# Performance work log

Hardware: AMD Instinct MI355X
Metric: run time of the kernel (lower is better)

## Reference

```python
import jax, jax.numpy as jnp
import numpy as np

N_NODES = 100000
N_EDGES = 1600000
D_IN = 128
D_OUT = 128
BN_EPS = 1e-5


def setup_inputs() -> dict:
    key = jax.random.key(0)
    ks = jax.random.split(key, 6)
    x = jax.random.normal(ks[0], (N_NODES, D_IN), dtype=jnp.float32)
    edge_index = jax.random.randint(ks[1], (2, N_EDGES), 0, N_NODES, dtype=jnp.int32)
    edge_weight = jax.random.uniform(ks[2], (N_EDGES,), dtype=jnp.float32)
    W = jax.random.normal(ks[3], (D_IN, D_OUT), dtype=jnp.float32) / np.sqrt(D_IN)
    b = jax.random.normal(ks[4], (D_OUT,), dtype=jnp.float32) * 0.01
    gamma = jnp.ones((D_OUT,), dtype=jnp.float32)
    beta = jnp.zeros((D_OUT,), dtype=jnp.float32)
    return {"x": x, "edge_index": edge_index, "edge_weight": edge_weight,
            "W": W, "b": b, "gamma": gamma, "beta": beta}


def reference(x, edge_index, edge_weight, W, b, gamma, beta):
    n = x.shape[0]
    # add self loops (add_self_loops=True)
    self_loops = jnp.arange(n, dtype=edge_index.dtype)
    row = jnp.concatenate([edge_index[0], self_loops])  # source
    col = jnp.concatenate([edge_index[1], self_loops])  # destination
    ew = jnp.concatenate([edge_weight, jnp.ones((n,), x.dtype)])
    # degree via scatter-add of ones on source nodes
    deg = jax.ops.segment_sum(jnp.ones_like(ew), row, num_segments=n)
    dinv = jnp.where(deg > 0, jax.lax.rsqrt(deg), 0.0)
    norm = dinv[row] * dinv[col] * ew  # [E+N]
    # linear transform
    h = x @ W + b  # [N, D_OUT]
    # per-edge gather -> scale -> scatter-add (vectorized form of the python loop)
    msgs = norm[:, None] * h[row]  # [E+N, D_OUT]
    out = jax.ops.segment_sum(msgs, col, num_segments=n)  # [N, D_OUT]
    # BatchNorm1d (training mode: biased batch stats)
    mean = jnp.mean(out, axis=0)
    var = jnp.mean(jnp.square(out - mean), axis=0)
    out = (out - mean) * jax.lax.rsqrt(var + BN_EPS) * gamma + beta
    return jax.nn.relu(out)
```

## Files before the change

kernel.cpp:

```cpp
#include <hip/hip_runtime.h>

#define DD 128
#define CAP 64
#define BINCAP 4608
#define S1_EPB 7168
#define DEG_R 16384
#define DEG_S 8

typedef __attribute__((ext_vector_type(8))) short short8;
typedef __attribute__((ext_vector_type(4))) float f32x4;

__device__ __forceinline__ unsigned short f2bf(float f) {
    unsigned int u; __builtin_memcpy(&u, &f, 4);
    unsigned int r = (u + 0x7FFFu + ((u >> 16) & 1u)) >> 16;
    return (unsigned short)r;
}
__device__ __forceinline__ unsigned int pack_bf(float a, float b) {
    return (unsigned int)f2bf(a) | ((unsigned int)f2bf(b) << 16);
}
__device__ __forceinline__ float lo_bf(unsigned int p) {
    unsigned int u = (p & 0xFFFFu) << 16; float f; __builtin_memcpy(&f, &u, 4); return f;
}
__device__ __forceinline__ float hi_bf(unsigned int p) {
    unsigned int u = p & 0xFFFF0000u; float f; __builtin_memcpy(&f, &u, 4); return f;
}
__device__ __forceinline__ float i2f(int v) { float f; __builtin_memcpy(&f, &v, 4); return f; }
__device__ __forceinline__ int f2i(float v) { int i; __builtin_memcpy(&i, &v, 4); return i; }

__global__ void k_init(int* deg, int* cursor, float* colsumR, float* colsumsqR, int N, int NBIN) {
    int i = blockIdx.x * 256 + threadIdx.x;
    if (i < N) deg[i] = 1;
    if (i < NBIN) cursor[i] = 0;
    if (i < 1024) { colsumR[i] = 0.0f; colsumsqR[i] = 0.0f; }
}

__global__ void k_wprep(const float* __restrict__ W, unsigned short* __restrict__ Wfrag) {
    int i = blockIdx.x * 256 + threadIdx.x;
    int k = i >> 7, n = i & 127;
    int tt = n >> 4, s = k >> 5, l = (((k >> 3) & 3) << 4) | (n & 15), j = k & 7;
    Wfrag[((tt * 4 + s) * 64 + l) * 8 + j] = f2bf(W[k * DD + n]);
}

__global__ __launch_bounds__(1024) void k_fused(
    const int* __restrict__ ei, const float* __restrict__ ew,
    int* __restrict__ deg, int* __restrict__ cursor, long long* __restrict__ coarse,
    int E, int N, int NBIN, int nS1i, int nDeg,
    const float* __restrict__ x, const unsigned short* __restrict__ Wfrag,
    const float* __restrict__ b, unsigned short* __restrict__ h)
{
    __shared__ int smem[16384];
    int t = threadIdx.x;
    int id = blockIdx.x;
    int role, rid;
    if (id < 2 * nS1i)           { role = (id & 1); rid = id >> 1; }
    else if (id < 2 * nS1i + nDeg) { role = 2; rid = id - 2 * nS1i; }
    else                         { role = 1; rid = nS1i + (id - 2 * nS1i - nDeg); }

    const int* row = ei;
    const int* col = ei + E;

    if (role == 0) {
        int* scnt  = smem;
        int* soff  = smem + 512;
        int* gbase = smem + 1024;
        long long* sorted = (long long*)(smem + 1536);
        for (int i = t; i < 512; i += 1024) scnt[i] = 0;
        __syncthreads();
        int e0 = rid * S1_EPB;
        int myrank[7];
#pragma unroll
        for (int j = 0; j < 7; ++j) {
            int e = e0 + j * 1024 + t;
            if (e < E) myrank[j] = atomicAdd(&scnt[col[e] >> 8], 1);
        }
        __syncthreads();
        if (t < 512) soff[t] = scnt[t];
        __syncthreads();
        for (int off = 1; off < 512; off <<= 1) {
            int v = 0;
            if (t < 512 && t >= off) v = soff[t - off];
            __syncthreads();
            if (t < 512) soff[t] += v;
            __syncthreads();
        }
        if (t < NBIN && scnt[t] > 0) gbase[t] = atomicAdd(&cursor[t], scnt[t]);
#pragma unroll
        for (int j = 0; j < 7; ++j) {
            int e = e0 + j * 1024 + t;
            if (e < E) {
                int c = col[e];
                int bn = c >> 8;
                int lo = row[e] | ((c & 255) << 17);
                long long ent = ((long long)(unsigned)f2i(ew[e]) << 32) | (unsigned)lo;
                sorted[(soff[bn] - scnt[bn]) + myrank[j]] = ent;
            }
        }
        __syncthreads();
        int wave = t >> 6, lane = t & 63;
        for (int bn = wave; bn < NBIN; bn += 16) {
            int k = scnt[bn];
            if (k == 0) continue;
            int off0 = soff[bn] - k;
            int gb = gbase[bn];
            long long* dst = coarse + (size_t)bn * BINCAP;
            for (int j = lane; j < k; j += 64) {
                int gp = gb + j;
                if (gp < BINCAP) dst[gp] = sorted[off0 + j];
            }
        }
        return;
    }
    if (role == 2) {
        int nr = (N + DEG_R - 1) / DEG_R;
        int ri = rid % nr, si = rid / nr;
        int* lc = smem;
        for (int i = t; i < DEG_R; i += 1024) lc[i] = 0;
        __syncthreads();
        int base = ri * DEG_R;
        int per = (E + DEG_S - 1) / DEG_S;
        int es = si * per, ee = es + per; if (ee > E) ee = E;
        int q0 = es >> 2, q1 = ee >> 2;
        const int4* r4 = (const int4*)row;
        for (int q = q0 + t; q < q1; q += 1024) {
            int4 v = r4[q];
            unsigned d0 = (unsigned)(v.x - base), d1 = (unsigned)(v.y - base);
            unsigned d2 = (unsigned)(v.z - base), d3 = (unsigned)(v.w - base);
            if (d0 < DEG_R) atomicAdd(&lc[d0], 1);
            if (d1 < DEG_R) atomicAdd(&lc[d1], 1);
            if (d2 < DEG_R) atomicAdd(&lc[d2], 1);
            if (d3 < DEG_R) atomicAdd(&lc[d3], 1);
        }
        for (int e = (q1 << 2) + t; e < ee; e += 1024) {
            unsigned d = (unsigned)(row[e] - base);
            if (d < DEG_R) atomicAdd(&lc[d], 1);
        }
        __syncthreads();
        for (int i = t; i < DEG_R; i += 1024) {
            int node = base + i, k = lc[i];
            if (node < N && k) atomicAdd(&deg[node], k);
        }
        return;
    }
    int lane = t & 63, wave = t >> 6;
    int row0 = rid * 256 + wave * 16;
    int mrow = row0 + (lane & 15);
    int kgrp = lane >> 4;
    f32x4 acc[8];
#pragma unroll
    for (int i = 0; i < 8; ++i) acc[i] = (f32x4){0.f, 0.f, 0.f, 0.f};
    const short8* Wf = (const short8*)Wfrag;
#pragma unroll
    for (int s = 0; s < 4; ++s) {
        float xv[8];
        if (mrow < N) {
            const float4* xp = (const float4*)(x + (size_t)mrow * DD + s * 32 + kgrp * 8);
            float4 xa = xp[0], xb = xp[1];
            xv[0] = xa.x; xv[1] = xa.y; xv[2] = xa.z; xv[3] = xa.w;
            xv[4] = xb.x; xv[5] = xb.y; xv[6] = xb.z; xv[7] = xb.w;
        } else {
#pragma unroll
            for (int j = 0; j < 8; ++j) xv[j] = 0.f;
        }
        short8 af;
#pragma unroll
        for (int j = 0; j < 8; ++j) af[j] = (short)f2bf(xv[j]);
#pragma unroll
        for (int tt = 0; tt < 8; ++tt) {
            short8 bf = Wf[(tt * 4 + s) * 64 + lane];
            acc[tt] = __builtin_amdgcn_mfma_f32_16x16x32_bf16(af, bf, acc[tt], 0, 0, 0);
        }
    }
    int drow = row0 + (lane >> 4) * 4;
    int coll = lane & 15;
#pragma unroll
    for (int tt = 0; tt < 8; ++tt) {
        int cc = tt * 16 + coll;
        float bias = b[cc];
#pragma unroll
        for (int rr = 0; rr < 4; ++rr) {
            int rw = drow + rr;
            if (rw < N) h[(size_t)rw * DD + cc] = f2bf(acc[tt][rr] + bias);
        }
    }
}

__global__ __launch_bounds__(1024) void k_stage2(
    const long long* __restrict__ coarse, const int* __restrict__ cursor,
    long long* __restrict__ bucket, int* __restrict__ cnt, int N)
{
    __shared__ int fcnt[256], fpos[256], fcur[256];
    __shared__ long long sorted2[BINCAP];
    int bn = blockIdx.x, t = threadIdx.x;
    int m = cursor[bn]; if (m > BINCAP) m = BINCAP;
    for (int i = t; i < 256; i += 1024) fcnt[i] = 0;
    __syncthreads();
    const long long* src = coarse + (size_t)bn * BINCAP;
    for (int i = t; i < m; i += 1024) {
        int lo = (int)src[i];
        atomicAdd(&fcnt[(lo >> 17) & 255], 1);
    }
    __syncthreads();
    if (t < 256) fpos[t] = fcnt[t];
    __syncthreads();
    for (int off = 1; off < 256; off <<= 1) {
        int v = 0;
        if (t < 256 && t >= off) v = fpos[t - off];
        __syncthreads();
        if (t < 256) fpos[t] += v;
        __syncthreads();
    }
    if (t < 256) fcur[t] = fpos[t] - fcnt[t];
    __syncthreads();
    for (int i = t; i < m; i += 1024) {
        long long v = src[i];
        int clo = ((int)v >> 17) & 255;
        int p = atomicAdd(&fcur[clo], 1);
        sorted2[p] = v;
    }
    __syncthreads();
    int wave = t >> 6, lane = t & 63;
    for (int d = wave; d < 256; d += 16) {
        int c = (bn << 8) + d;
        if (c >= N) continue;
        int k = fcnt[d]; if (k > CAP) k = CAP;
        int off0 = fpos[d] - fcnt[d];
        for (int j = lane; j < k; j += 64)
            bucket[(size_t)c * CAP + j] = sorted2[off0 + j];
    }
    if (t < 256) {
        int c = (bn << 8) + t;
        if (c < N) { int k = fcnt[t]; cnt[c] = (k > CAP) ? CAP : k; }
    }
}

__global__ __launch_bounds__(1024) void k_aggregate(
    const unsigned int* __restrict__ h, const int* __restrict__ cnt,
    const int2* __restrict__ bucket, const int* __restrict__ deg,
    unsigned int* __restrict__ outb, float* __restrict__ colsumR,
    float* __restrict__ colsumsqR, int N)
{
    __shared__ float ls[2048], lq[2048];
    int t = threadIdx.x, wave = t >> 6, lane = t & 63;
    int gw = blockIdx.x * 16 + wave;
    float s0 = 0, s1 = 0, q0 = 0, q1 = 0;
    for (int n = gw; n < N; n += 512 * 16) {
        float dn = rsqrtf((float)deg[n]);
        unsigned int p = h[(size_t)n * 64 + lane];
        float a0 = dn * lo_bf(p), a1 = dn * hi_bf(p);
        int cn = cnt[n];
        const int2* bk = bucket + (size_t)n * CAP;
        int j = 0;
        for (; j + 8 <= cn; j += 8) {
            int2 d0 = bk[j],     d1 = bk[j + 1], d2 = bk[j + 2], d3 = bk[j + 3];
            int2 d4 = bk[j + 4], d5 = bk[j + 5], d6 = bk[j + 6], d7 = bk[j + 7];
            int s0_ = d0.x & 0x1FFFF, s1_ = d1.x & 0x1FFFF, s2_ = d2.x & 0x1FFFF, s3_ = d3.x & 0x1FFFF;
            int s4_ = d4.x & 0x1FFFF, s5_ = d5.x & 0x1FFFF, s6_ = d6.x & 0x1FFFF, s7_ = d7.x & 0x1FFFF;
            unsigned int g0 = h[(size_t)s0_ * 64 + lane];
            unsigned int g1 = h[(size_t)s1_ * 64 + lane];
            unsigned int g2 = h[(size_t)s2_ * 64 + lane];
            unsigned int g3 = h[(size_t)s3_ * 64 + lane];
            unsigned int g4 = h[(size_t)s4_ * 64 + lane];
            unsigned int g5 = h[(size_t)s5_ * 64 + lane];
            unsigned int g6 = h[(size_t)s6_ * 64 + lane];
            unsigned int g7 = h[(size_t)s7_ * 64 + lane];
            float w0 = rsqrtf((float)deg[s0_]) * i2f(d0.y), w1 = rsqrtf((float)deg[s1_]) * i2f(d1.y);
            float w2 = rsqrtf((float)deg[s2_]) * i2f(d2.y), w3 = rsqrtf((float)deg[s3_]) * i2f(d3.y);
            float w4 = rsqrtf((float)deg[s4_]) * i2f(d4.y), w5 = rsqrtf((float)deg[s5_]) * i2f(d5.y);
            float w6 = rsqrtf((float)deg[s6_]) * i2f(d6.y), w7 = rsqrtf((float)deg[s7_]) * i2f(d7.y);
            a0 = fmaf(w0, lo_bf(g0), a0); a1 = fmaf(w0, hi_bf(g0), a1);
            a0 = fmaf(w1, lo_bf(g1), a0); a1 = fmaf(w1, hi_bf(g1), a1);
            a0 = fmaf(w2, lo_bf(g2), a0); a1 = fmaf(w2, hi_bf(g2), a1);
            a0 = fmaf(w3, lo_bf(g3), a0); a1 = fmaf(w3, hi_bf(g3), a1);
            a0 = fmaf(w4, lo_bf(g4), a0); a1 = fmaf(w4, hi_bf(g4), a1);
            a0 = fmaf(w5, lo_bf(g5), a0); a1 = fmaf(w5, hi_bf(g5), a1);
            a0 = fmaf(w6, lo_bf(g6), a0); a1 = fmaf(w6, hi_bf(g6), a1);
            a0 = fmaf(w7, lo_bf(g7), a0); a1 = fmaf(w7, hi_bf(g7), a1);
        }
        for (; j < cn; ++j) {
            int2 d = bk[j];
            int sr = d.x & 0x1FFFF;
            unsigned int g = h[(size_t)sr * 64 + lane];
            float w = rsqrtf((float)deg[sr]) * i2f(d.y);
            a0 = fmaf(w, lo_bf(g), a0);
            a1 = fmaf(w, hi_bf(g), a1);
        }
        a0 *= dn; a1 *= dn;
        outb[(size_t)n * 64 + lane] = pack_bf(a0, a1);
        s0 += a0; q0 += a0 * a0;
        s1 += a1; q1 += a1 * a1;
    }
    ls[wave * 128 + lane * 2] = s0; ls[wave * 128 + lane * 2 + 1] = s1;
    lq[wave * 128 + lane * 2] = q0; lq[wave * 128 + lane * 2 + 1] = q1;
    __syncthreads();
    if (t < 128) {
        float S = 0, Q = 0;
#pragma unroll
        for (int w = 0; w < 16; ++w) { S += ls[w * 128 + t]; Q += lq[w * 128 + t]; }
        int rep = (blockIdx.x & 7) * 128 + t;
        atomicAdd(&colsumR[rep], S);
        atomicAdd(&colsumsqR[rep], Q);
    }
}

__global__ void k_bn_final(const float* __restrict__ colsumR, const float* __restrict__ colsumsqR,
                           const float* __restrict__ gamma, const float* __restrict__ beta,
                           float* __restrict__ ss, int N) {
    int c = threadIdx.x;
    float S = 0, Q = 0;
#pragma unroll
    for (int r = 0; r < 8; ++r) { S += colsumR[r * 128 + c]; Q += colsumsqR[r * 128 + c]; }
    float invN = 1.0f / (float)N;
    float mean = S * invN;
    float var = Q * invN - mean * mean;
    float inv = rsqrtf(var + 1e-5f);
    float sc = gamma[c] * inv;
    ss[c] = sc;
    ss[128 + c] = beta[c] - mean * sc;
}

__global__ __launch_bounds__(256) void k_bn_apply(const unsigned int* __restrict__ outb,
                                                  float* __restrict__ out,
                                                  const float* __restrict__ ss, int total64) {
    int i = blockIdx.x * 256 + threadIdx.x;
    if (i >= total64) return;
    int c0 = (i & 63) * 2;
    unsigned int p = outb[i];
    float v0 = fmaxf(lo_bf(p) * ss[c0]     + ss[128 + c0],     0.0f);
    float v1 = fmaxf(hi_bf(p) * ss[c0 + 1] + ss[128 + c0 + 1], 0.0f);
    ((float2*)out)[i] = make_float2(v0, v1);
}

extern "C" void kernel_launch(void* const* d_in, const int* in_sizes, int n_in,
                              void* d_out, int out_size, void* d_ws, size_t ws_size,
                              hipStream_t stream) {
    const float* x     = (const float*)d_in[0];
    const int* ei      = (const int*)d_in[1];
    const float* ew    = (const float*)d_in[2];
    const float* W     = (const float*)d_in[3];
    const float* b     = (const float*)d_in[4];
    const float* gamma = (const float*)d_in[5];
    const float* beta  = (const float*)d_in[6];
    float* out = (float*)d_out;

    int N = in_sizes[0] / DD;
    int E = in_sizes[2];
    int NBIN = (N + 255) / 256;

    char* wsb = (char*)d_ws;
    size_t off = 0;
    auto alloc = [&](size_t bytes) -> char* {
        char* p = wsb + off;
        off = (off + bytes + 255) & ~(size_t)255;
        return p;
    };
    int* deg        = (int*)alloc((size_t)N * 4);
    int* cnt        = (int*)alloc((size_t)N * 4);
    int* cursor     = (int*)alloc((size_t)NBIN * 4);
    long long* coarse = (long long*)alloc((size_t)NBIN * BINCAP * 8);
    long long* bucket = (long long*)alloc((size_t)N * CAP * 8);
    unsigned short* h = (unsigned short*)alloc((size_t)N * DD * 2);
    unsigned short* Wfrag = (unsigned short*)alloc(DD * DD * 2);
    unsigned int* outb = (unsigned int*)alloc((size_t)N * 64 * 4);
    float* colsumR   = (float*)alloc(1024 * 4);
    float* colsumsqR = (float*)alloc(1024 * 4);
    float* ss        = (float*)alloc(256 * 4);

    int nS1   = (E + S1_EPB - 1) / S1_EPB;
    int nGemm = (N + 255) / 256;
    int nS1i  = (nS1 < nGemm) ? nS1 : nGemm;
    int nDeg  = ((N + DEG_R - 1) / DEG_R) * DEG_S;
    int GF    = 2 * nS1i + nDeg + (nGemm - nS1i);

    k_init<<<dim3((N + 255) / 256), dim3(256), 0, stream>>>(deg, cursor, colsumR, colsumsqR, N, NBIN);
    k_wprep<<<dim3(64), dim3(256), 0, stream>>>(W, Wfrag);
    k_fused<<<dim3(GF), dim3(1024), 0, stream>>>(ei, ew, deg, cursor, coarse, E, N, NBIN,
                                                 nS1i, nDeg, x, Wfrag, b, h);
    k_stage2<<<dim3(NBIN), dim3(1024), 0, stream>>>(coarse, cursor, bucket, cnt, N);
    k_aggregate<<<dim3(512), dim3(1024), 0, stream>>>((const unsigned int*)h, cnt,
                                                      (const int2*)bucket, deg,
                                                      outb, colsumR, colsumsqR, N);
    k_bn_final<<<dim3(1), dim3(128), 0, stream>>>(colsumR, colsumsqR, gamma, beta, ss, N);
    k_bn_apply<<<dim3((N * 64 + 255) / 256), dim3(256), 0, stream>>>(outb, out, ss, N * 64);
}
```

Measured before the change: 272.9 us.

## Fuse bin sort into aggregation, precompute edge norms, merge prep and BN kernels

The second-stage bin sort now feeds aggregation directly from shared memory, so the per-node bucket array is no longer written to and reread from global memory. The full edge normalisation is computed once per edge during the sort, and the per-node CAP truncation is gone. The init and W-prep kernels are merged into one, as are BN finalize and apply, cutting launch count. In exchange, aggregation parallelism drops to one block per 256-node bin, about 391 blocks, and each block uses much more shared memory, which may lower occupancy and worsen load balance.

```diff
diff --git a/kernel.cpp b/kernel.cpp
--- a/kernel.cpp
+++ b/kernel.cpp
@@ -1,7 +1,6 @@
 #include <hip/hip_runtime.h>
 
 #define DD 128
-#define CAP 64
 #define BINCAP 4608
 #define S1_EPB 7168
 #define DEG_R 16384
@@ -27,15 +26,17 @@
 __device__ __forceinline__ float i2f(int v) { float f; __builtin_memcpy(&f, &v, 4); return f; }
 __device__ __forceinline__ int f2i(float v) { int i; __builtin_memcpy(&i, &v, 4); return i; }
 
-__global__ void k_init(int* deg, int* cursor, float* colsumR, float* colsumsqR, int N, int NBIN) {
-    int i = blockIdx.x * 256 + threadIdx.x;
-    if (i < N) deg[i] = 1;
-    if (i < NBIN) cursor[i] = 0;
-    if (i < 1024) { colsumR[i] = 0.0f; colsumsqR[i] = 0.0f; }
-}
-
-__global__ void k_wprep(const float* __restrict__ W, unsigned short* __restrict__ Wfrag) {
-    int i = blockIdx.x * 256 + threadIdx.x;
+__global__ void k_prep(int* deg, int* cursor, float* colsumR, float* colsumsqR, int N, int NBIN,
+                       int nInit, const float* __restrict__ W, unsigned short* __restrict__ Wfrag) {
+    int bid = blockIdx.x, t = threadIdx.x;
+    if (bid < nInit) {
+        int i = bid * 256 + t;
+        if (i < N) deg[i] = 1;
+        if (i < NBIN) cursor[i] = 0;
+        if (i < 1024) { colsumR[i] = 0.0f; colsumsqR[i] = 0.0f; }
+        return;
+    }
+    int i = (bid - nInit) * 256 + t;
     int k = i >> 7, n = i & 127;
     int tt = n >> 4, s = k >> 5, l = (((k >> 3) & 3) << 4) | (n & 15), j = k & 7;
     Wfrag[((tt * 4 + s) * 64 + l) * 8 + j] = f2bf(W[k * DD + n]);
@@ -184,12 +185,15 @@
     }
 }
 
-__global__ __launch_bounds__(1024) void k_stage2(
+__global__ __launch_bounds__(1024) void k_agg(
     const long long* __restrict__ coarse, const int* __restrict__ cursor,
-    long long* __restrict__ bucket, int* __restrict__ cnt, int N)
+    const int* __restrict__ deg, const unsigned int* __restrict__ h,
+    unsigned int* __restrict__ outb, float* __restrict__ colsumR,
+    float* __restrict__ colsumsqR, int N)
 {
+    __shared__ long long sorted2[BINCAP];
     __shared__ int fcnt[256], fpos[256], fcur[256];
-    __shared__ long long sorted2[BINCAP];
+    __shared__ float ls[2048], lq[2048];
     int bn = blockIdx.x, t = threadIdx.x;
     int m = cursor[bn]; if (m > BINCAP) m = BINCAP;
     for (int i = t; i < 256; i += 1024) fcnt[i] = 0;
@@ -213,60 +217,43 @@
     __syncthreads();
     for (int i = t; i < m; i += 1024) {
         long long v = src[i];
-        int clo = ((int)v >> 17) & 255;
+        int lo = (int)v;
+        int clo = (lo >> 17) & 255;
+        int sr = lo & 0x1FFFF;
+        int c = (bn << 8) + clo;
+        float w = rsqrtf((float)deg[sr]) * rsqrtf((float)deg[c]) * i2f((int)(v >> 32));
         int p = atomicAdd(&fcur[clo], 1);
-        sorted2[p] = v;
+        sorted2[p] = ((long long)(unsigned)f2i(w) << 32) | (unsigned)sr;
     }
     __syncthreads();
     int wave = t >> 6, lane = t & 63;
+    float s0 = 0, s1 = 0, q0 = 0, q1 = 0;
+    const int2* sp = (const int2*)sorted2;
     for (int d = wave; d < 256; d += 16) {
         int c = (bn << 8) + d;
         if (c >= N) continue;
-        int k = fcnt[d]; if (k > CAP) k = CAP;
-        int off0 = fpos[d] - fcnt[d];
-        for (int j = lane; j < k; j += 64)
-            bucket[(size_t)c * CAP + j] = sorted2[off0 + j];
-    }
-    if (t < 256) {
-        int c = (bn << 8) + t;
-        if (c < N) { int k = fcnt[t]; cnt[c] = (k > CAP) ? CAP : k; }
-    }
-}
-
-__global__ __launch_bounds__(1024) void k_aggregate(
-    const unsigned int* __restrict__ h, const int* __restrict__ cnt,
-    const int2* __restrict__ bucket, const int* __restrict__ deg,
-    unsigned int* __restrict__ outb, float* __restrict__ colsumR,
-    float* __restrict__ colsumsqR, int N)
-{
-    __shared__ float ls[2048], lq[2048];
-    int t = threadIdx.x, wave = t >> 6, lane = t & 63;
-    int gw = blockIdx.x * 16 + wave;
-    float s0 = 0, s1 = 0, q0 = 0, q1 = 0;
-    for (int n = gw; n < N; n += 512 * 16) {
-        float dn = rsqrtf((float)deg[n]);
-        unsigned int p = h[(size_t)n * 64 + lane];
-        float a0 = dn * lo_bf(p), a1 = dn * hi_bf(p);
-        int cn = cnt[n];
-        const int2* bk = bucket + (size_t)n * CAP;
+        float dn = rsqrtf((float)deg[c]);
+        float sn = dn * dn;
+        unsigned int p = h[(size_t)c * 64 + lane];
+        float a0 = sn * lo_bf(p), a1 = sn * hi_bf(p);
+        int cn = fcnt[d];
+        int off0 = fpos[d] - cn;
         int j = 0;
         for (; j + 8 <= cn; j += 8) {
-            int2 d0 = bk[j],     d1 = bk[j + 1], d2 = bk[j + 2], d3 = bk[j + 3];
-            int2 d4 = bk[j + 4], d5 = bk[j + 5], d6 = bk[j + 6], d7 = bk[j + 7];
-            int s0_ = d0.x & 0x1FFFF, s1_ = d1.x & 0x1FFFF, s2_ = d2.x & 0x1FFFF, s3_ = d3.x & 0x1FFFF;
-            int s4_ = d4.x & 0x1FFFF, s5_ = d5.x & 0x1FFFF, s6_ = d6.x & 0x1FFFF, s7_ = d7.x & 0x1FFFF;
-            unsigned int g0 = h[(size_t)s0_ * 64 + lane];
-            unsigned int g1 = h[(size_t)s1_ * 64 + lane];
-            unsigned int g2 = h[(size_t)s2_ * 64 + lane];
-            unsigned int g3 = h[(size_t)s3_ * 64 + lane];
-            unsigned int g4 = h[(size_t)s4_ * 64 + lane];
-            unsigned int g5 = h[(size_t)s5_ * 64 + lane];
-            unsigned int g6 = h[(size_t)s6_ * 64 + lane];
-            unsigned int g7 = h[(size_t)s7_ * 64 + lane];
-            float w0 = rsqrtf((float)deg[s0_]) * i2f(d0.y), w1 = rsqrtf((float)deg[s1_]) * i2f(d1.y);
-            float w2 = rsqrtf((float)deg[s2_]) * i2f(d2.y), w3 = rsqrtf((float)deg[s3_]) * i2f(d3.y);
-            float w4 = rsqrtf((float)deg[s4_]) * i2f(d4.y), w5 = rsqrtf((float)deg[s5_]) * i2f(d5.y);
-            float w6 = rsqrtf((float)deg[s6_]) * i2f(d6.y), w7 = rsqrtf((float)deg[s7_]) * i2f(d7.y);
+            int2 d0 = sp[off0 + j],     d1 = sp[off0 + j + 1];
+            int2 d2 = sp[off0 + j + 2], d3 = sp[off0 + j + 3];
+            int2 d4 = sp[off0 + j + 4], d5 = sp[off0 + j + 5];
+            int2 d6 = sp[off0 + j + 6], d7 = sp[off0 + j + 7];
+            unsigned int g0 = h[(size_t)d0.x * 64 + lane];
+            unsigned int g1 = h[(size_t)d1.x * 64 + lane];
+            unsigned int g2 = h[(size_t)d2.x * 64 + lane];
+            unsigned int g3 = h[(size_t)d3.x * 64 + lane];
+            unsigned int g4 = h[(size_t)d4.x * 64 + lane];
+            unsigned int g5 = h[(size_t)d5.x * 64 + lane];
+            unsigned int g6 = h[(size_t)d6.x * 64 + lane];
+            unsigned int g7 = h[(size_t)d7.x * 64 + lane];
+            float w0 = i2f(d0.y), w1 = i2f(d1.y), w2 = i2f(d2.y), w3 = i2f(d3.y);
+            float w4 = i2f(d4.y), w5 = i2f(d5.y), w6 = i2f(d6.y), w7 = i2f(d7.y);
             a0 = fmaf(w0, lo_bf(g0), a0); a1 = fmaf(w0, hi_bf(g0), a1);
             a0 = fmaf(w1, lo_bf(g1), a0); a1 = fmaf(w1, hi_bf(g1), a1);
             a0 = fmaf(w2, lo_bf(g2), a0); a1 = fmaf(w2, hi_bf(g2), a1);
@@ -277,15 +264,13 @@
             a0 = fmaf(w7, lo_bf(g7), a0); a1 = fmaf(w7, hi_bf(g7), a1);
         }
         for (; j < cn; ++j) {
-            int2 d = bk[j];
-            int sr = d.x & 0x1FFFF;
-            unsigned int g = h[(size_t)sr * 64 + lane];
-            float w = rsqrtf((float)deg[sr]) * i2f(d.y);
+            int2 dd = sp[off0 + j];
+            unsigned int g = h[(size_t)dd.x * 64 + lane];
+            float w = i2f(dd.y);
             a0 = fmaf(w, lo_bf(g), a0);
             a1 = fmaf(w, hi_bf(g), a1);
         }
-        a0 *= dn; a1 *= dn;
-        outb[(size_t)n * 64 + lane] = pack_bf(a0, a1);
+        outb[(size_t)c * 64 + lane] = pack_bf(a0, a1);
         s0 += a0; q0 += a0 * a0;
         s1 += a1; q1 += a1 * a1;
     }
@@ -296,38 +281,40 @@
         float S = 0, Q = 0;
 #pragma unroll
         for (int w = 0; w < 16; ++w) { S += ls[w * 128 + t]; Q += lq[w * 128 + t]; }
-        int rep = (blockIdx.x & 7) * 128 + t;
+        int rep = (bn & 7) * 128 + t;
         atomicAdd(&colsumR[rep], S);
         atomicAdd(&colsumsqR[rep], Q);
     }
 }
 
-__global__ void k_bn_final(const float* __restrict__ colsumR, const float* __restrict__ colsumsqR,
-                           const float* __restrict__ gamma, const float* __restrict__ beta,
-                           float* __restrict__ ss, int N) {
-    int c = threadIdx.x;
-    float S = 0, Q = 0;
-#pragma unroll
-    for (int r = 0; r < 8; ++r) { S += colsumR[r * 128 + c]; Q += colsumsqR[r * 128 + c]; }
-    float invN = 1.0f / (float)N;
-    float mean = S * invN;
-    float var = Q * invN - mean * mean;
-    float inv = rsqrtf(var + 1e-5f);
-    float sc = gamma[c] * inv;
-    ss[c] = sc;
-    ss[128 + c] = beta[c] - mean * sc;
-}
-
-__global__ __launch_bounds__(256) void k_bn_apply(const unsigned int* __restrict__ outb,
-                                                  float* __restrict__ out,
-                                                  const float* __restrict__ ss, int total64) {
-    int i = blockIdx.x * 256 + threadIdx.x;
-    if (i >= total64) return;
-    int c0 = (i & 63) * 2;
-    unsigned int p = outb[i];
-    float v0 = fmaxf(lo_bf(p) * ss[c0]     + ss[128 + c0],     0.0f);
-    float v1 = fmaxf(hi_bf(p) * ss[c0 + 1] + ss[128 + c0 + 1], 0.0f);
-    ((float2*)out)[i] = make_float2(v0, v1);
+__global__ __launch_bounds__(256) void k_bn(
+    const unsigned int* __restrict__ outb, float* __restrict__ out,
+    const float* __restrict__ colsumR, const float* __restrict__ colsumsqR,
+    const float* __restrict__ gamma, const float* __restrict__ beta,
+    int N, int total64)
+{
+    __shared__ float ss[256];
+    int t = threadIdx.x;
+    if (t < 128) {
+        float S = 0, Q = 0;
+#pragma unroll
+        for (int r = 0; r < 8; ++r) { S += colsumR[r * 128 + t]; Q += colsumsqR[r * 128 + t]; }
+        float invN = 1.0f / (float)N;
+        float mean = S * invN;
+        float var = Q * invN - mean * mean;
+        float inv = rsqrtf(var + 1e-5f);
+        float sc = gamma[t] * inv;
+        ss[t] = sc;
+        ss[128 + t] = beta[t] - mean * sc;
+    }
+    __syncthreads();
+    for (int i = blockIdx.x * 256 + t; i < total64; i += gridDim.x * 256) {
+        int c0 = (i & 63) * 2;
+        unsigned int p = outb[i];
+        float v0 = fmaxf(lo_bf(p) * ss[c0]     + ss[128 + c0],     0.0f);
+        float v1 = fmaxf(hi_bf(p) * ss[c0 + 1] + ss[128 + c0 + 1], 0.0f);
+        ((float2*)out)[i] = make_float2(v0, v1);
+    }
 }
 
 extern "C" void kernel_launch(void* const* d_in, const int* in_sizes, int n_in,
@@ -354,31 +341,27 @@
         return p;
     };
     int* deg        = (int*)alloc((size_t)N * 4);
-    int* cnt        = (int*)alloc((size_t)N * 4);
     int* cursor     = (int*)alloc((size_t)NBIN * 4);
     long long* coarse = (long long*)alloc((size_t)NBIN * BINCAP * 8);
-    long long* bucket = (long long*)alloc((size_t)N * CAP * 8);
     unsigned short* h = (unsigned short*)alloc((size_t)N * DD * 2);
     unsigned short* Wfrag = (unsigned short*)alloc(DD * DD * 2);
     unsigned int* outb = (unsigned int*)alloc((size_t)N * 64 * 4);
     float* colsumR   = (float*)alloc(1024 * 4);
     float* colsumsqR = (float*)alloc(1024 * 4);
-    float* ss        = (float*)alloc(256 * 4);
-
+
+    int nInit = (N + 255) / 256;
     int nS1   = (E + S1_EPB - 1) / S1_EPB;
     int nGemm = (N + 255) / 256;
     int nS1i  = (nS1 < nGemm) ? nS1 : nGemm;
     int nDeg  = ((N + DEG_R - 1) / DEG_R) * DEG_S;
     int GF    = 2 * nS1i + nDeg + (nGemm - nS1i);
 
-    k_init<<<dim3((N + 255) / 256), dim3(256), 0, stream>>>(deg, cursor, colsumR, colsumsqR, N, NBIN);
-    k_wprep<<<dim3(64), dim3(256), 0, stream>>>(W, Wfrag);
+    k_prep<<<dim3(nInit + 64), dim3(256), 0, stream>>>(deg, cursor, colsumR, colsumsqR,
+                                                       N, NBIN, nInit, W, Wfrag);
     k_fused<<<dim3(GF), dim3(1024), 0, stream>>>(ei, ew, deg, cursor, coarse, E, N, NBIN,
                                                  nS1i, nDeg, x, Wfrag, b, h);
-    k_stage2<<<dim3(NBIN), dim3(1024), 0, stream>>>(coarse, cursor, bucket, cnt, N);
-    k_aggregate<<<dim3(512), dim3(1024), 0, stream>>>((const unsigned int*)h, cnt,
-                                                      (const int2*)bucket, deg,
-                                                      outb, colsumR, colsumsqR, N);
-    k_bn_final<<<dim3(1), dim3(128), 0, stream>>>(colsumR, colsumsqR, gamma, beta, ss, N);
-    k_bn_apply<<<dim3((N * 64 + 255) / 256), dim3(256), 0, stream>>>(outb, out, ss, N * 64);
-}
+    k_agg<<<dim3(NBIN), dim3(1024), 0, stream>>>(coarse, cursor, deg, (const unsigned int*)h,
+                                                 outb, colsumR, colsumsqR, N);
+    k_bn<<<dim3(2048), dim3(256), 0, stream>>>(outb, out, colsumR, colsumsqR,
+                                               gamma, beta, N, N * 64);
+}
```

Result: faster. 236.7 us (-13.3%).
